# Kernel tuning notes

Hardware: AMD Instinct MI355X
Metric: run time of the kernel (lower is better)

Reference implementation:

```python
import jax, jax.numpy as jnp
import numpy as np

SIGNAL_LEN = 2048
N_WAVELETS = 32
TWO_PI = 2.0 * np.pi


def _encoder(x, W1, b1, W2, b2, W3, b3, W4, b4):
    B = x.shape[0]
    h = x.reshape(B, -1)                      # (B, 4096)
    h = jax.nn.relu(h @ W1.T + b1)            # (B, 1024)
    h = jax.nn.relu(h @ W2.T + b2)            # (B, 512)
    h = jax.nn.relu(h @ W3.T + b3)            # (B, 256)
    return h @ W4.T + b4                      # (B, n_wavelets*5)


def _synthesize(params):
    # params: (B, N_WAVELETS, 5)
    A = params[..., 0]                                    # (B, N)
    t0 = jax.nn.sigmoid(params[..., 1]) * SIGNAL_LEN      # (B, N)
    f = jax.nn.sigmoid(params[..., 2]) * 0.5              # (B, N)
    sigma = jax.nn.sigmoid(params[..., 3]) * 200.0 + 2.0  # (B, N)
    phi = params[..., 4]                                  # (B, N)

    t = jnp.arange(SIGNAL_LEN, dtype=params.dtype)        # (T,)
    dt = t[None, None, :] - t0[..., None]                 # (B, N, T)
    g = (A[..., None]
         * jnp.exp(-(dt * dt) / (2.0 * sigma[..., None] ** 2))
         * jnp.cos(TWO_PI * f[..., None] * dt + phi[..., None]))  # (B, N, T)
    sig = jnp.sum(g, axis=1)                              # (B, T)
    # both channels receive the identical wavelet sum (as in the torch code)
    return jnp.stack([sig, sig], axis=1)                  # (B, 2, T)


def setup_inputs() -> dict:
    key = jax.random.key(0)
    ks = jax.random.split(key, 9)
    B = 4096
    def w(k, shape, fan_in):
        return jax.random.normal(k, shape, dtype=jnp.float32) / np.sqrt(fan_in)
    return {
        "x": jax.random.normal(ks[0], (B, 2, SIGNAL_LEN), dtype=jnp.float32),
        "W1": w(ks[1], (1024, 4096), 4096), "b1": jnp.zeros((1024,), jnp.float32),
        "W2": w(ks[2], (512, 1024), 1024),  "b2": jnp.zeros((512,), jnp.float32),
        "W3": w(ks[3], (256, 512), 512),    "b3": jnp.zeros((256,), jnp.float32),
        "W4": w(ks[4], (N_WAVELETS * 5, 256), 256), "b4": jnp.zeros((N_WAVELETS * 5,), jnp.float32),
    }


def reference(x, W1, b1, W2, b2, W3, b3, W4, b4):
    B = x.shape[0]
    params = _encoder(x, W1, b1, W2, b2, W3, b3, W4, b4).reshape(B, N_WAVELETS, 5)
    return _synthesize(params)  # (B, 2, SIGNAL_LEN)
```

## Files before the change

### kernel.cpp

```cpp
#include <hip/hip_runtime.h>


#define SIGNAL_LEN 2048
#define NWAV 32

typedef _Float16 f16x8 __attribute__((ext_vector_type(8)));
typedef _Float16 f16x4 __attribute__((ext_vector_type(4)));
typedef float    f32x4 __attribute__((ext_vector_type(4)));

__device__ __forceinline__ void load16_lds(const _Float16* g, _Float16* l) {
  __builtin_amdgcn_global_load_lds((const __attribute__((address_space(1))) void*)g,
                                   (__attribute__((address_space(3))) void*)l,
                                   16, 0, 0);
}

struct HL { _Float16 h, l; };
__device__ __forceinline__ HL split_one(float a) {
  HL r;
  r.h = (_Float16)a;
  r.l = (_Float16)((a - (float)r.h) * 4096.0f);
  return r;
}

__global__ void split_x(const float4* __restrict__ src, f16x4* __restrict__ dh,
                        f16x4* __restrict__ dl) {
  int i = blockIdx.x * 256 + threadIdx.x;
  float4 v = src[i];
  float a[4] = {v.x, v.y, v.z, v.w};
  f16x4 h, l;
#pragma unroll
  for (int j = 0; j < 4; j++) {
    HL r = split_one(a[j]);
    h[j] = r.h;
    l[j] = r.l;
  }
  dh[i] = h;
  dl[i] = l;
}

__global__ void split_weights(const float* __restrict__ W1, const float* __restrict__ W2,
                              const float* __restrict__ W3, const float* __restrict__ W4,
                              const float* __restrict__ b4,
                              f16x4* __restrict__ W1h, f16x4* __restrict__ W1l,
                              f16x4* __restrict__ W2h, f16x4* __restrict__ W2l,
                              f16x4* __restrict__ W3h, f16x4* __restrict__ W3l,
                              f16x4* __restrict__ W4h, f16x4* __restrict__ W4l,
                              float* __restrict__ b4p) {
  const int blk = blockIdx.x;
  const int tid = threadIdx.x;
  if (blk < 4736) {
    const float4* src;
    f16x4 *dh, *dl;
    int i;
    if (blk < 4096) {
      src = (const float4*)W1; dh = W1h; dl = W1l; i = blk * 256 + tid;
    } else if (blk < 4608) {
      src = (const float4*)W2; dh = W2h; dl = W2l; i = (blk - 4096) * 256 + tid;
    } else {
      src = (const float4*)W3; dh = W3h; dl = W3l; i = (blk - 4608) * 256 + tid;
    }
    float4 v = src[i];
    float a[4] = {v.x * 256.0f, v.y * 256.0f, v.z * 256.0f, v.w * 256.0f};
    f16x4 h, l;
#pragma unroll
    for (int j = 0; j < 4; j++) {
      HL r = split_one(a[j]);
      h[j] = r.h;
      l[j] = r.l;
    }
    dh[i] = h;
    dl[i] = l;
  } else if (blk < 4800) {
    int i = (blk - 4736) * 256 + tid;
    int i4 = i << 2;
    int row = i4 >> 8;
    f16x4 h, l;
#pragma unroll
    for (int j = 0; j < 4; j++) {
      float a = (row < 160) ? W4[i4 + j] * 256.0f : 0.0f;
      HL r = split_one(a);
      h[j] = r.h;
      l[j] = r.l;
    }
    W4h[i] = h;
    W4l[i] = l;
  } else {
    b4p[tid] = (tid < 160) ? b4[tid] : 0.0f;
  }
}

template <int TM, int TN, int N, int K, bool RELU, bool SPLIT_OUT>
__global__ void __launch_bounds__(256, 2)
gemm_fused(const _Float16* __restrict__ Ah, const _Float16* __restrict__ Al,
           const _Float16* __restrict__ Bh, const _Float16* __restrict__ Bl,
           const float* __restrict__ bias,
           _Float16* __restrict__ Ch, _Float16* __restrict__ Cl,
           float* __restrict__ Cf) {
  constexpr int AM = TM / 32;
  constexpr int BN = TN / 32;
  constexpr int AU = TM / 8;
  constexpr int TU = (TM + TN) / 8;
  constexpr int UPW = TU / 4;
  constexpr int NK = K / 32;

  __shared__ __align__(16) _Float16 s[2][(TM + TN) * 64];

  const int tid = threadIdx.x;
  const int lane = tid & 63;
  const int w = tid >> 6;
  const int wm = w >> 1, wn = w & 1;
  const int m0 = blockIdx.y * TM;
  const int n0 = blockIdx.x * TN;

  const int srow = lane >> 2;
  const int sk8 = (((lane & 3) - (lane >> 3)) & 3) * 8;

  const _Float16* gb[UPW];
  int lo[UPW];
#pragma unroll
  for (int i = 0; i < UPW; ++i) {
    const int u = w * UPW + i;
    if (u < AU) {
      const int g = u >> 1, hl = u & 1;
      gb[i] = (hl ? Al : Ah) + (size_t)(m0 + g * 16 + srow) * K + sk8;
    } else {
      const int ub = u - AU;
      const int g = ub >> 1, hl = ub & 1;
      gb[i] = (hl ? Bl : Bh) + (size_t)(n0 + g * 16 + srow) * K + sk8;
    }
    lo[i] = u * 512;
  }

  const int fr = lane & 15;
  const int fq = lane >> 4;
  const int fslot8 = (4 * fr + ((fq + (fr >> 1)) & 3)) * 8;

  f32x4 acc1[AM][BN], acc2[AM][BN];
#pragma unroll
  for (int i = 0; i < AM; i++)
#pragma unroll
    for (int j = 0; j < BN; j++) {
      acc1[i][j] = 0.0f;
      acc2[i][j] = 0.0f;
    }

#pragma unroll
  for (int i = 0; i < UPW; ++i) load16_lds(gb[i], &s[0][lo[i]]);

  for (int kt = 0; kt < NK; ++kt) {
    const int cur = kt & 1;
    __syncthreads();

    if (kt + 1 < NK) {
      const int kofs = (kt + 1) * 32;
#pragma unroll
      for (int i = 0; i < UPW; ++i) load16_lds(gb[i] + kofs, &s[cur ^ 1][lo[i]]);
    }

    f16x8 fAh[AM], fAl[AM], fBh[BN], fBl[BN];
#pragma unroll
    for (int im = 0; im < AM; ++im) {
      const int g = wm * AM + im;
      fAh[im] = *(const f16x8*)(&s[cur][(g * 2 + 0) * 512 + fslot8]);
      fAl[im] = *(const f16x8*)(&s[cur][(g * 2 + 1) * 512 + fslot8]);
    }
#pragma unroll
    for (int in = 0; in < BN; ++in) {
      const int g = wn * BN + in;
      fBh[in] = *(const f16x8*)(&s[cur][TM * 64 + (g * 2 + 0) * 512 + fslot8]);
      fBl[in] = *(const f16x8*)(&s[cur][TM * 64 + (g * 2 + 1) * 512 + fslot8]);
    }
#pragma unroll
    for (int im = 0; im < AM; ++im) {
#pragma unroll
      for (int in = 0; in < BN; ++in) {
        acc1[im][in] = __builtin_amdgcn_mfma_f32_16x16x32_f16(fAh[im], fBh[in], acc1[im][in], 0, 0, 0);
        acc2[im][in] = __builtin_amdgcn_mfma_f32_16x16x32_f16(fAh[im], fBl[in], acc2[im][in], 0, 0, 0);
        acc2[im][in] = __builtin_amdgcn_mfma_f32_16x16x32_f16(fAl[im], fBh[in], acc2[im][in], 0, 0, 0);
      }
    }
  }

  const int quad = lane >> 4;
#pragma unroll
  for (int in = 0; in < BN; ++in) {
    const int n = n0 + wn * (TN / 2) + in * 16 + fr;
    const float bv = bias[n];
#pragma unroll
    for (int im = 0; im < AM; ++im) {
#pragma unroll
      for (int r = 0; r < 4; ++r) {
        const int m = m0 + wm * (TM / 2) + im * 16 + quad * 4 + r;
        float c = (acc1[im][in][r] + acc2[im][in][r] * (1.0f / 4096.0f)) * (1.0f / 256.0f) + bv;
        if (RELU) c = fmaxf(c, 0.0f);
        const size_t off = (size_t)m * N + n;
        if (SPLIT_OUT) {
          HL rr = split_one(c);
          Ch[off] = rr.h;
          Cl[off] = rr.l;
        } else {
          Cf[off] = c;
        }
      }
    }
  }
}

template <int TM, int TN, int N, int K, int KSPLIT, int MINW>
__global__ void __launch_bounds__(256, MINW)
gemm_part(const _Float16* __restrict__ Ah, const _Float16* __restrict__ Al,
          const _Float16* __restrict__ Bh, const _Float16* __restrict__ Bl,
          float* __restrict__ Cp) {
  constexpr int AM = TM / 32;
  constexpr int BN = TN / 32;
  constexpr int AU = TM / 8;
  constexpr int TU = (TM + TN) / 8;
  constexpr int UPW = TU / 4;
  constexpr int NK = K / KSPLIT / 32;

  __shared__ __align__(16) _Float16 s[2][(TM + TN) * 64];

  const int tid = threadIdx.x;
  const int lane = tid & 63;
  const int w = tid >> 6;
  const int wm = w >> 1, wn = w & 1;
  const int m0 = blockIdx.y * TM;
  const int n0 = blockIdx.x * TN;
  const int kb = blockIdx.z * (K / KSPLIT);

  const int srow = lane >> 2;
  const int sk8 = (((lane & 3) - (lane >> 3)) & 3) * 8;

  const _Float16* gb[UPW];
  int lo[UPW];
#pragma unroll
  for (int i = 0; i < UPW; ++i) {
    const int u = w * UPW + i;
    if (u < AU) {
      const int g = u >> 1, hl = u & 1;
      gb[i] = (hl ? Al : Ah) + (size_t)(m0 + g * 16 + srow) * K + kb + sk8;
    } else {
      const int ub = u - AU;
      const int g = ub >> 1, hl = ub & 1;
      gb[i] = (hl ? Bl : Bh) + (size_t)(n0 + g * 16 + srow) * K + kb + sk8;
    }
    lo[i] = u * 512;
  }

  const int fr = lane & 15;
  const int fq = lane >> 4;
  const int fslot8 = (4 * fr + ((fq + (fr >> 1)) & 3)) * 8;

  f32x4 acc1[AM][BN], acc2[AM][BN];
#pragma unroll
  for (int i = 0; i < AM; i++)
#pragma unroll
    for (int j = 0; j < BN; j++) {
      acc1[i][j] = 0.0f;
      acc2[i][j] = 0.0f;
    }

#pragma unroll
  for (int i = 0; i < UPW; ++i) load16_lds(gb[i], &s[0][lo[i]]);

  for (int kt = 0; kt < NK; ++kt) {
    const int cur = kt & 1;
    __syncthreads();

    if (kt + 1 < NK) {
      const int kofs = (kt + 1) * 32;
#pragma unroll
      for (int i = 0; i < UPW; ++i) load16_lds(gb[i] + kofs, &s[cur ^ 1][lo[i]]);
    }

    f16x8 fAh[AM], fAl[AM], fBh[BN], fBl[BN];
#pragma unroll
    for (int im = 0; im < AM; ++im) {
      const int g = wm * AM + im;
      fAh[im] = *(const f16x8*)(&s[cur][(g * 2 + 0) * 512 + fslot8]);
      fAl[im] = *(const f16x8*)(&s[cur][(g * 2 + 1) * 512 + fslot8]);
    }
#pragma unroll
    for (int in = 0; in < BN; ++in) {
      const int g = wn * BN + in;
      fBh[in] = *(const f16x8*)(&s[cur][TM * 64 + (g * 2 + 0) * 512 + fslot8]);
      fBl[in] = *(const f16x8*)(&s[cur][TM * 64 + (g * 2 + 1) * 512 + fslot8]);
    }
#pragma unroll
    for (int im = 0; im < AM; ++im) {
#pragma unroll
      for (int in = 0; in < BN; ++in) {
        acc1[im][in] = __builtin_amdgcn_mfma_f32_16x16x32_f16(fAh[im], fBh[in], acc1[im][in], 0, 0, 0);
        acc2[im][in] = __builtin_amdgcn_mfma_f32_16x16x32_f16(fAh[im], fBl[in], acc2[im][in], 0, 0, 0);
        acc2[im][in] = __builtin_amdgcn_mfma_f32_16x16x32_f16(fAl[im], fBh[in], acc2[im][in], 0, 0, 0);
      }
    }
  }

  const int quad = lane >> 4;
  float* Cz = Cp + (size_t)blockIdx.z * ((size_t)gridDim.y * TM) * N;
#pragma unroll
  for (int in = 0; in < BN; ++in) {
    const int n = n0 + wn * (TN / 2) + in * 16 + fr;
#pragma unroll
    for (int im = 0; im < AM; ++im) {
#pragma unroll
      for (int r = 0; r < 4; ++r) {
        const int m = m0 + wm * (TM / 2) + im * 16 + quad * 4 + r;
        Cz[(size_t)m * N + n] = acc1[im][in][r] + acc2[im][in][r] * (1.0f / 4096.0f);
      }
    }
  }
}

__global__ void __launch_bounds__(256)
combine1(const float* __restrict__ Cp, const float* __restrict__ bias, int N,
         size_t halfN, _Float16* __restrict__ Ch, _Float16* __restrict__ Cl) {
  const size_t i4 = ((size_t)blockIdx.x * 256 + threadIdx.x) * 4;
  float4 p0 = *(const float4*)(Cp + i4);
  float4 p1 = *(const float4*)(Cp + halfN + i4);
  float4 bv = *(const float4*)(bias + (i4 % (size_t)N));
  float c[4] = {(p0.x + p1.x) * (1.0f / 256.0f) + bv.x,
                (p0.y + p1.y) * (1.0f / 256.0f) + bv.y,
                (p0.z + p1.z) * (1.0f / 256.0f) + bv.z,
                (p0.w + p1.w) * (1.0f / 256.0f) + bv.w};
  f16x4 h, l;
#pragma unroll
  for (int j = 0; j < 4; j++) {
    c[j] = fmaxf(c[j], 0.0f);
    HL r = split_one(c[j]);
    h[j] = r.h;
    l[j] = r.l;
  }
  *(f16x4*)(Ch + i4) = h;
  *(f16x4*)(Cl + i4) = l;
}

__global__ void __launch_bounds__(256)
synth(const float* __restrict__ P, float* __restrict__ out) {
  __shared__ float sA[NWAV], sT0[NWAV], sF[NWAV], sC[NWAV], sPh[NWAV], sSg[NWAV];
  const int b = blockIdx.x;
  const int tid = threadIdx.x;
  if (tid < NWAV) {
    const float* q = P + (size_t)b * 256 + tid * 5;
    const float L2E = 1.44269504088896340736f;
    float A = q[0], p1 = q[1], p2 = q[2], p3 = q[3], p4 = q[4];
    float s1 = 1.0f / (1.0f + exp2f(-p1 * L2E));
    float s2 = 1.0f / (1.0f + exp2f(-p2 * L2E));
    float s3 = 1.0f / (1.0f + exp2f(-p3 * L2E));
    float sg = s3 * 200.0f + 2.0f;
    sA[tid] = A;
    sT0[tid] = s1 * 2048.0f;
    sF[tid] = s2 * 0.5f;
    sC[tid] = -L2E / (2.0f * sg * sg);
    sPh[tid] = p4 * 0.15915494309189535f;
    sSg[tid] = sg;
  }
  __syncthreads();

  const float t0f = (float)(tid * 8);
  const int wlo = (tid & ~63) * 8;
  float acc[8];
#pragma unroll
  for (int i = 0; i < 8; i++) acc[i] = 0.0f;

  for (int wv = 0; wv < NWAV; wv++) {
    const float t0 = sT0[wv], sg = sSg[wv];
    if (t0 + 5.0f * sg < (float)wlo || t0 - 5.0f * sg > (float)(wlo + 511)) continue;
    const float A = sA[wv], fr = sF[wv], cn = sC[wv], ph = sPh[wv];
#pragma unroll
    for (int i = 0; i < 8; i++) {
      float dt = (t0f + (float)i) - t0;
      float e = exp2f(dt * dt * cn);
      float r = fr * dt + ph;
      r -= floorf(r);
      float cs = __builtin_amdgcn_cosf(r);
      acc[i] += A * e * cs;
    }
  }

  float* o = out + (size_t)b * (2 * SIGNAL_LEN) + tid * 8;
  float4 v0 = make_float4(acc[0], acc[1], acc[2], acc[3]);
  float4 v1 = make_float4(acc[4], acc[5], acc[6], acc[7]);
  *(float4*)(o) = v0;
  *(float4*)(o + 4) = v1;
  *(float4*)(o + SIGNAL_LEN) = v0;
  *(float4*)(o + SIGNAL_LEN + 4) = v1;
}

extern "C" void kernel_launch(void* const* d_in, const int* in_sizes, int n_in,
                              void* d_out, int out_size, void* d_ws, size_t ws_size,
                              hipStream_t stream) {
  (void)in_sizes; (void)n_in; (void)out_size; (void)ws_size;
  const float* X  = (const float*)d_in[0];
  const float* W1 = (const float*)d_in[1];
  const float* b1 = (const float*)d_in[2];
  const float* W2 = (const float*)d_in[3];
  const float* b2 = (const float*)d_in[4];
  const float* W3 = (const float*)d_in[5];
  const float* b3 = (const float*)d_in[6];
  const float* W4 = (const float*)d_in[7];
  const float* b4 = (const float*)d_in[8];
  float* out = (float*)d_out;

  char* p = (char*)d_ws;
  auto take = [&](size_t bytes) -> char* {
    char* r = p;
    p += (bytes + 255) & ~(size_t)255;
    return r;
  };
  _Float16* Xh  = (_Float16*)take((size_t)4096 * 4096 * 2);
  _Float16* Xl  = (_Float16*)take((size_t)4096 * 4096 * 2);
  _Float16* W1h = (_Float16*)take((size_t)1024 * 4096 * 2);
  _Float16* W1l = (_Float16*)take((size_t)1024 * 4096 * 2);
  _Float16* H1h = (_Float16*)take((size_t)4096 * 1024 * 2);
  _Float16* H1l = (_Float16*)take((size_t)4096 * 1024 * 2);
  _Float16* W2h = (_Float16*)take((size_t)512 * 1024 * 2);
  _Float16* W2l = (_Float16*)take((size_t)512 * 1024 * 2);
  _Float16* H2h = (_Float16*)take((size_t)4096 * 512 * 2);
  _Float16* H2l = (_Float16*)take((size_t)4096 * 512 * 2);
  _Float16* W3h = (_Float16*)take((size_t)256 * 512 * 2);
  _Float16* W3l = (_Float16*)take((size_t)256 * 512 * 2);
  _Float16* H3h = (_Float16*)take((size_t)4096 * 256 * 2);
  _Float16* H3l = (_Float16*)take((size_t)4096 * 256 * 2);
  _Float16* W4h = (_Float16*)take((size_t)256 * 256 * 2);
  _Float16* W4l = (_Float16*)take((size_t)256 * 256 * 2);
  float*    b4p = (float*)take(256 * 4);
  float*    Pp  = (float*)take((size_t)4096 * 256 * 4);
  float*    Cp  = (float*)take((size_t)2 * 4096 * 1024 * 4);

  split_x<<<16384, 256, 0, stream>>>((const float4*)X, (f16x4*)Xh, (f16x4*)Xl);
  split_weights<<<4801, 256, 0, stream>>>(W1, W2, W3, W4, b4,
                                          (f16x4*)W1h, (f16x4*)W1l, (f16x4*)W2h, (f16x4*)W2l,
                                          (f16x4*)W3h, (f16x4*)W3l, (f16x4*)W4h, (f16x4*)W4l, b4p);

  gemm_part<128, 256, 1024, 4096, 2, 1><<<dim3(4, 32, 2), 256, 0, stream>>>(
      Xh, Xl, W1h, W1l, Cp);
  combine1<<<4096, 256, 0, stream>>>(Cp, b1, 1024, (size_t)4096 * 1024, H1h, H1l);

  gemm_fused<64, 128, 512, 1024, true, true><<<dim3(4, 64), 256, 0, stream>>>(
      H1h, H1l, W2h, W2l, b2, H2h, H2l, nullptr);
  gemm_fused<64, 64, 256, 512, true, true><<<dim3(4, 64), 256, 0, stream>>>(
      H2h, H2l, W3h, W3l, b3, H3h, H3l, nullptr);
  gemm_fused<64, 64, 256, 256, false, false><<<dim3(4, 64), 256, 0, stream>>>(
      H3h, H3l, W4h, W4l, b4p, nullptr, nullptr, Pp);

  synth<<<4096, 256, 0, stream>>>(Pp, out);
}
```

Before: 404.3 us.

## Load W1 fragments directly from global into registers in the first GEMM

The first-layer split-K GEMM now stages only the activation tile in LDS. Each wave reads its own slice of the W1 high/low fragments straight from global memory into registers, and waves are split along N only rather than 2x2. The aim is to cut LDS traffic and shared memory use, and to double A-fragment reuse per wave. In exchange, B is read from global without coalescing or double buffering, the per-wave accumulator count doubles (AM=8, BN=4), and register pressure rises.

```diff
diff --git a/kernel.cpp b/kernel.cpp
--- a/kernel.cpp
+++ b/kernel.cpp
@@ -206,24 +206,22 @@
   }
 }
 
-template <int TM, int TN, int N, int K, int KSPLIT, int MINW>
-__global__ void __launch_bounds__(256, MINW)
-gemm_part(const _Float16* __restrict__ Ah, const _Float16* __restrict__ Al,
-          const _Float16* __restrict__ Bh, const _Float16* __restrict__ Bl,
-          float* __restrict__ Cp) {
-  constexpr int AM = TM / 32;
-  constexpr int BN = TN / 32;
+template <int TM, int TN, int N, int K, int KSPLIT>
+__global__ void __launch_bounds__(256, 1)
+gemm_g1(const _Float16* __restrict__ Ah, const _Float16* __restrict__ Al,
+        const _Float16* __restrict__ Bh, const _Float16* __restrict__ Bl,
+        float* __restrict__ Cp) {
+  constexpr int AM = TM / 16;
+  constexpr int BN = TN / 4 / 16;
   constexpr int AU = TM / 8;
-  constexpr int TU = (TM + TN) / 8;
-  constexpr int UPW = TU / 4;
+  constexpr int UPW = AU / 4;
   constexpr int NK = K / KSPLIT / 32;
 
-  __shared__ __align__(16) _Float16 s[2][(TM + TN) * 64];
+  __shared__ __align__(16) _Float16 s[2][AU * 512];
 
   const int tid = threadIdx.x;
   const int lane = tid & 63;
   const int w = tid >> 6;
-  const int wm = w >> 1, wn = w & 1;
   const int m0 = blockIdx.y * TM;
   const int n0 = blockIdx.x * TN;
   const int kb = blockIdx.z * (K / KSPLIT);
@@ -236,14 +234,8 @@
 #pragma unroll
   for (int i = 0; i < UPW; ++i) {
     const int u = w * UPW + i;
-    if (u < AU) {
-      const int g = u >> 1, hl = u & 1;
-      gb[i] = (hl ? Al : Ah) + (size_t)(m0 + g * 16 + srow) * K + kb + sk8;
-    } else {
-      const int ub = u - AU;
-      const int g = ub >> 1, hl = ub & 1;
-      gb[i] = (hl ? Bl : Bh) + (size_t)(n0 + g * 16 + srow) * K + kb + sk8;
-    }
+    const int g = u >> 1, hl = u & 1;
+    gb[i] = (hl ? Al : Ah) + (size_t)(m0 + g * 16 + srow) * K + kb + sk8;
     lo[i] = u * 512;
   }
 
@@ -251,6 +243,9 @@
   const int fq = lane >> 4;
   const int fslot8 = (4 * fr + ((fq + (fr >> 1)) & 3)) * 8;
 
+  const _Float16* Bhb = Bh + (size_t)(n0 + w * (TN / 4) + fr) * K + kb + fq * 8;
+  const _Float16* Blb = Bl + (size_t)(n0 + w * (TN / 4) + fr) * K + kb + fq * 8;
+
   f32x4 acc1[AM][BN], acc2[AM][BN];
 #pragma unroll
   for (int i = 0; i < AM; i++)
@@ -267,24 +262,25 @@
     const int cur = kt & 1;
     __syncthreads();
 
+    f16x8 fBh[BN], fBl[BN];
+#pragma unroll
+    for (int in = 0; in < BN; ++in) {
+      const size_t bo = (size_t)in * 16 * K + kt * 32;
+      fBh[in] = *(const f16x8*)(Bhb + bo);
+      fBl[in] = *(const f16x8*)(Blb + bo);
+    }
+
     if (kt + 1 < NK) {
       const int kofs = (kt + 1) * 32;
 #pragma unroll
       for (int i = 0; i < UPW; ++i) load16_lds(gb[i] + kofs, &s[cur ^ 1][lo[i]]);
     }
 
-    f16x8 fAh[AM], fAl[AM], fBh[BN], fBl[BN];
-#pragma unroll
-    for (int im = 0; im < AM; ++im) {
-      const int g = wm * AM + im;
-      fAh[im] = *(const f16x8*)(&s[cur][(g * 2 + 0) * 512 + fslot8]);
-      fAl[im] = *(const f16x8*)(&s[cur][(g * 2 + 1) * 512 + fslot8]);
-    }
-#pragma unroll
-    for (int in = 0; in < BN; ++in) {
-      const int g = wn * BN + in;
-      fBh[in] = *(const f16x8*)(&s[cur][TM * 64 + (g * 2 + 0) * 512 + fslot8]);
-      fBl[in] = *(const f16x8*)(&s[cur][TM * 64 + (g * 2 + 1) * 512 + fslot8]);
+    f16x8 fAh[AM], fAl[AM];
+#pragma unroll
+    for (int im = 0; im < AM; ++im) {
+      fAh[im] = *(const f16x8*)(&s[cur][(im * 2 + 0) * 512 + fslot8]);
+      fAl[im] = *(const f16x8*)(&s[cur][(im * 2 + 1) * 512 + fslot8]);
     }
 #pragma unroll
     for (int im = 0; im < AM; ++im) {
@@ -301,12 +297,12 @@
   float* Cz = Cp + (size_t)blockIdx.z * ((size_t)gridDim.y * TM) * N;
 #pragma unroll
   for (int in = 0; in < BN; ++in) {
-    const int n = n0 + wn * (TN / 2) + in * 16 + fr;
+    const int n = n0 + w * (TN / 4) + in * 16 + fr;
 #pragma unroll
     for (int im = 0; im < AM; ++im) {
 #pragma unroll
       for (int r = 0; r < 4; ++r) {
-        const int m = m0 + wm * (TM / 2) + im * 16 + quad * 4 + r;
+        const int m = m0 + im * 16 + quad * 4 + r;
         Cz[(size_t)m * N + n] = acc1[im][in][r] + acc2[im][in][r] * (1.0f / 4096.0f);
       }
     }
@@ -434,7 +430,7 @@
                                           (f16x4*)W1h, (f16x4*)W1l, (f16x4*)W2h, (f16x4*)W2l,
                                           (f16x4*)W3h, (f16x4*)W3l, (f16x4*)W4h, (f16x4*)W4l, b4p);
 
-  gemm_part<128, 256, 1024, 4096, 2, 1><<<dim3(4, 32, 2), 256, 0, stream>>>(
+  gemm_g1<128, 256, 1024, 4096, 2><<<dim3(4, 32, 2), 256, 0, stream>>>(
       Xh, Xl, W1h, W1l, Cp);
   combine1<<<4096, 256, 0, stream>>>(Cp, b1, 1024, (size_t)4096 * 1024, H1h, H1l);
 
```

After: 453.0 us. 1.12x slower.
